# Performance work log

Hardware: AMD Instinct MI355X
Metric: run time of the kernel (lower is better)

## Reference

```python
import jax, jax.numpy as jnp
import numpy as np

B, N, D, P = 32, 16, 64, 8  # batch, num_objs, in_feat_dim, patch size
PAIRS = N * (N - 1)


def _conv_relu(x, W, b):
    # Conv2d(kernel=3, stride=1, padding=1) + ReLU, NCHW/OIHW layout
    y = jax.lax.conv_general_dilated(
        x, W, window_strides=(1, 1), padding='SAME',
        dimension_numbers=('NCHW', 'OIHW', 'NCHW'))
    return jax.nn.relu(y + b[None, :, None, None])


def setup_inputs() -> dict:
    key = jax.random.key(0)
    ks = jax.random.split(key, 12)
    x = jax.random.normal(ks[0], (B, N, D, P, P), jnp.float32)
    # g_idx: cols 0,1 index into the repeated pair axis of size N*(N-1); col 2 is a 0/1 mask
    i0 = jax.random.randint(ks[1], (B, PAIRS, 1), 0, PAIRS)
    i1 = jax.random.randint(ks[2], (B, PAIRS, 1), 0, PAIRS)
    m = jax.random.randint(ks[3], (B, PAIRS, 1), 0, 2)
    g_idx = jnp.concatenate([i0, i1, m], axis=2)

    def w(k, o, i):
        return jax.random.normal(k, (o, i, 3, 3), jnp.float32) * (1.0 / np.sqrt(i * 9.0))

    return {
        'x': x, 'g_idx': g_idx,
        'W_rel': w(ks[4], D, 2 * D), 'b_rel': jnp.zeros((D,), jnp.float32),
        'W_self': w(ks[5], D, D), 'b_self': jnp.zeros((D,), jnp.float32),
        'W_aff': w(ks[6], D, D), 'b_aff': jnp.zeros((D,), jnp.float32),
        'W_agg': w(ks[7], D, 2 * D), 'b_agg': jnp.zeros((D,), jnp.float32),
    }


def reference(x, g_idx, W_rel, b_rel, W_self, b_self, W_aff, b_aff, W_agg, b_agg):
    b, n, d, p, _ = x.shape
    pairs = n * (n - 1)
    s = x
    # x1: [B, N*(N-1), D, P, P]
    x1 = jnp.tile(x, (1, n - 1, 1, 1, 1))

    def gather_pair(col):
        idx = g_idx[:, :, col][:, :, None, None, None]  # [B, pairs, 1, 1, 1]
        idx = jnp.broadcast_to(idx, (b, pairs, d, p, p))
        return jnp.take_along_axis(x1, idx, axis=1)

    y1 = gather_pair(0)
    y2 = gather_pair(1)
    mask = g_idx[:, :, 2][:, :, None, None, None].astype(x.dtype)
    r = jnp.concatenate([y1, y2], axis=2) * mask  # [B, pairs, 2D, P, P]
    r = _conv_relu(r.reshape(-1, 2 * d, p, p), W_rel, b_rel)
    r = r.reshape(b, n, n - 1, d, p, p).sum(axis=2)  # scatter-sum per object

    xs = _conv_relu(x.reshape(-1, d, p, p), W_self, b_self).reshape(b, n, d, p, p)
    pred = xs + r
    a = _conv_relu(pred.reshape(-1, d, p, p), W_aff, b_aff).reshape(b, n, d, p, p)
    a = jnp.concatenate([a, s], axis=2)  # [B, N, 2D, P, P]
    out = _conv_relu(a.reshape(-1, 2 * d, p, p), W_agg, b_agg).reshape(b, n, d, p, p)
    return out
```

## Files before the change

kernel.cpp:

```cpp
#include <hip/hip_runtime.h>


#define NIMG 512
#define IMGSZ 4096

using bf16x8 = __attribute__((ext_vector_type(8))) short;
using f32x4  = __attribute__((ext_vector_type(4))) float;
using u16x8  = __attribute__((ext_vector_type(8))) unsigned short;

__device__ inline unsigned short f2bf(float f) {
  union { float f; unsigned u; } v; v.f = f;
  unsigned r = v.u + 0x7fffu + ((v.u >> 16) & 1u);
  return (unsigned short)(r >> 16);
}

__global__ __launch_bounds__(256) void prep(
    const float* __restrict__ x,
    const float* __restrict__ Wr, const float* __restrict__ Ws,
    const float* __restrict__ Wa, const float* __restrict__ Wg,
    unsigned short* __restrict__ xt, unsigned short* __restrict__ Wt)
{
  const int blk = blockIdx.x;
  if (blk < 512) {
    __shared__ __align__(16) unsigned short st[64 * 68];
    const int tid = threadIdx.x, w = tid >> 6, lane = tid & 63;
    const float* base = x + (size_t)blk * IMGSZ;
    const int px = lane;
#pragma unroll
    for (int r = 0; r < 8; ++r) {
      int ic0 = (w + 4 * r) * 2;
      const float* s = base + ic0 * 64;
      float a = s[px], c = s[64 + px];
      *(unsigned*)(st + px * 68 + ic0) = (unsigned)f2bf(a) | ((unsigned)f2bf(c) << 16);
    }
    __syncthreads();
    const int row = tid >> 2;
#pragma unroll
    for (int k = 0; k < 2; ++k) {
      int c = (tid & 3) * 2 + k;
      *(u16x8*)(xt + (size_t)blk * IMGSZ + row * 64 + c * 8) =
          *(const u16x8*)(st + row * 68 + c * 8);
    }
  } else {
    int idx = (blk - 512) * 256 + threadIdx.x;
    if (idx >= 221184) return;
    float v;
    if (idx < 73728) {
      int c = idx / 36864, r = idx % 36864;
      int t = r >> 12, oc = (r >> 6) & 63, ic = r & 63;
      v = (c == 0 ? Ws : Wa)[oc * 576 + ic * 9 + t];
    } else {
      int r2 = idx - 73728;
      int half = r2 / 73728, rr = r2 % 73728;
      int t = rr >> 13, oc = (rr >> 7) & 63, ic = rr & 127;
      v = (half ? Wg : Wr)[oc * 1152 + ic * 9 + t];
    }
    Wt[idx] = f2bf(v);
  }
}

__device__ inline void decode_img(int j, int& b, int& o) {
  b = ((j >> 7) << 3) | (j & 7);
  o = (j >> 3) & 15;
}

__global__ __launch_bounds__(256) void k1(
    const unsigned short* __restrict__ xt,
    const unsigned short* __restrict__ Wt,
    const float* __restrict__ b_self,
    float* __restrict__ xs, float* __restrict__ cA, float* __restrict__ cB)
{
  constexpr int ROW = 72;
  __shared__ __align__(16) unsigned short sX[65 * ROW];
  int b, o;
  decode_img(blockIdx.x, b, o);
  const int img = b * 16 + o;
  const int tid = threadIdx.x;
  const int w = tid >> 6, lane = tid & 63;

  {
    const unsigned short* xo = xt + (size_t)img * IMGSZ;
    const int row = tid >> 2, c = tid & 3;
    *(u16x8*)(sX + row * ROW + c * 16)     = *(const u16x8*)(xo + row * 64 + c * 16);
    *(u16x8*)(sX + row * ROW + c * 16 + 8) = *(const u16x8*)(xo + row * 64 + c * 16 + 8);
  }
  if (tid < 36) ((unsigned*)(sX + 64 * ROW))[tid] = 0;
  __syncthreads();

  const int q = lane >> 4, n16 = lane & 15;
  const int ocb = w * 16;
  const int co = ocb + q * 4;
  const int aw64 = (ocb + n16) * 64 + q * 8;

  int pyt[4], pxt[4];
#pragma unroll
  for (int t = 0; t < 4; ++t) { int p = t * 16 + n16; pyt[t] = p >> 3; pxt[t] = p & 7; }

  f32x4 aS[4] = {}, aA[4] = {}, aB[4] = {};
  const unsigned short* WS = Wt + aw64;
  const unsigned short* WA = Wt + 73728 + (ocb + n16) * 128 + q * 8;
  const unsigned short* WB = WA + 64;
#pragma unroll
  for (int tap = 0; tap < 9; ++tap) {
    const int dy = tap / 3 - 1, dx = tap % 3 - 1;
    int spt[4];
#pragma unroll
    for (int t = 0; t < 4; ++t) {
      int sy = pyt[t] + dy, sx = pxt[t] + dx;
      spt[t] = ((unsigned)sy < 8u && (unsigned)sx < 8u) ? (sy * 8 + sx) : 64;
    }
#pragma unroll
    for (int ks = 0; ks < 2; ++ks) {
      bf16x8 as = *(const bf16x8*)(WS + tap * 4096 + ks * 32);
      bf16x8 aa = *(const bf16x8*)(WA + tap * 8192 + ks * 32);
      bf16x8 ab = *(const bf16x8*)(WB + tap * 8192 + ks * 32);
#pragma unroll
      for (int t = 0; t < 4; ++t) {
        bf16x8 bt = *(const bf16x8*)(sX + spt[t] * ROW + ks * 32 + q * 8);
        aS[t] = __builtin_amdgcn_mfma_f32_16x16x32_bf16(as, bt, aS[t], 0, 0, 0);
        aA[t] = __builtin_amdgcn_mfma_f32_16x16x32_bf16(aa, bt, aA[t], 0, 0, 0);
        aB[t] = __builtin_amdgcn_mfma_f32_16x16x32_bf16(ab, bt, aB[t], 0, 0, 0);
      }
    }
  }

  const size_t ib = (size_t)img * IMGSZ;
#pragma unroll
  for (int t = 0; t < 4; ++t) {
    int p = t * 16 + n16;
    f32x4 vs = aS[t];
#pragma unroll
    for (int r = 0; r < 4; ++r) vs[r] = fmaxf(vs[r] + b_self[co + r], 0.f);
    *(f32x4*)(xs + ib + p * 64 + co) = vs;
    *(f32x4*)(cA + ib + p * 64 + co) = aA[t];
    *(f32x4*)(cB + ib + p * 64 + co) = aB[t];
  }
}

__global__ __launch_bounds__(256, 2) void k2(
    const unsigned short* __restrict__ xt,
    const int* __restrict__ g_idx,
    const unsigned short* __restrict__ Wt,
    const float* __restrict__ b_rel, const float* __restrict__ b_aff,
    const float* __restrict__ b_agg,
    const float* __restrict__ xs, const float* __restrict__ cA,
    const float* __restrict__ cB,
    float* __restrict__ out)
{
  constexpr int ROW = 72, ROW2 = 136;
  __shared__ __align__(16) unsigned short sX[65 * ROW2];
  __shared__ __align__(16) unsigned short sPred[65 * ROW];
  __shared__ int so1[15], so2[15];
  __shared__ float sm[15];

  int b, i;
  decode_img(blockIdx.x, b, i);
  const int img = b * 16 + i;
  const int tid = threadIdx.x;
  const int w = tid >> 6, lane = tid & 63;

  if (tid < 15) {
    const int* gp = g_idx + ((size_t)b * 240 + i * 15 + tid) * 3;
    so1[tid] = gp[0] & 15;
    so2[tid] = gp[1] & 15;
    sm[tid]  = (float)gp[2];
  }

  {
    const unsigned short* xo = xt + (size_t)img * IMGSZ;
    const int row = tid >> 2, c = tid & 3;
    *(u16x8*)(sX + row * ROW2 + 64 + c * 16)     = *(const u16x8*)(xo + row * 64 + c * 16);
    *(u16x8*)(sX + row * ROW2 + 64 + c * 16 + 8) = *(const u16x8*)(xo + row * 64 + c * 16 + 8);
  }
  if (tid < 68) ((unsigned*)(sX + 64 * ROW2))[tid] = 0;
  if (tid < 36) ((unsigned*)(sPred + 64 * ROW))[tid] = 0;
  __syncthreads();

  {
    const size_t bb = (size_t)b * 16 * IMGSZ;
    const float* xbase = xs + (size_t)img * IMGSZ;
#pragma unroll 1
    for (int pass = 0; pass < 4; ++pass) {
      const int e = tid * 4 + pass * 1024;
      const int e_px = e >> 6, e_ic = e & 63;
      f32x4 v1[15], v2[15];
#pragma unroll
      for (int j = 0; j < 15; ++j) {
        v1[j] = *(const f32x4*)(cA + bb + (size_t)so1[j] * IMGSZ + e);
        v2[j] = *(const f32x4*)(cB + bb + (size_t)so2[j] * IMGSZ + e);
      }
      f32x4 xv = *(const f32x4*)(xbase + e);
      float acc[4], br[4];
#pragma unroll
      for (int r = 0; r < 4; ++r) { br[r] = b_rel[e_ic + r]; acc[r] = xv[r]; }
#pragma unroll
      for (int j = 0; j < 15; ++j) {
        float m = sm[j];
#pragma unroll
        for (int r = 0; r < 4; ++r)
          acc[r] += fmaxf(m * (v1[j][r] + v2[j][r]) + br[r], 0.f);
      }
      uint2 pk;
      pk.x = (unsigned)f2bf(acc[0]) | ((unsigned)f2bf(acc[1]) << 16);
      pk.y = (unsigned)f2bf(acc[2]) | ((unsigned)f2bf(acc[3]) << 16);
      *(uint2*)(sPred + e_px * ROW + e_ic) = pk;
    }
  }
  __syncthreads();

  const int q = lane >> 4, n16 = lane & 15;
  const int ocb = w * 16;
  const int co = ocb + q * 4;
  const int aw64  = (ocb + n16) * 64 + q * 8;
  const int aw128 = (ocb + n16) * 128 + q * 8;

  int pyt[4], pxt[4];
#pragma unroll
  for (int t = 0; t < 4; ++t) { int p = t * 16 + n16; pyt[t] = p >> 3; pxt[t] = p & 7; }

  {
    f32x4 f[4] = {};
    const unsigned short* WA = Wt + 36864 + aw64;
#pragma unroll
    for (int tap = 0; tap < 9; ++tap) {
      const int dy = tap / 3 - 1, dx = tap % 3 - 1;
      int spt[4];
#pragma unroll
      for (int t = 0; t < 4; ++t) {
        int sy = pyt[t] + dy, sx = pxt[t] + dx;
        spt[t] = ((unsigned)sy < 8u && (unsigned)sx < 8u) ? (sy * 8 + sx) : 64;
      }
#pragma unroll
      for (int ks = 0; ks < 2; ++ks) {
        bf16x8 a = *(const bf16x8*)(WA + tap * 4096 + ks * 32);
#pragma unroll
        for (int t = 0; t < 4; ++t) {
          bf16x8 bt = *(const bf16x8*)(sPred + spt[t] * ROW + ks * 32 + q * 8);
          f[t] = __builtin_amdgcn_mfma_f32_16x16x32_bf16(a, bt, f[t], 0, 0, 0);
        }
      }
    }
#pragma unroll
    for (int t = 0; t < 4; ++t) {
      int p = t * 16 + n16;
      float v0 = fmaxf(f[t][0] + b_aff[co + 0], 0.f);
      float v1 = fmaxf(f[t][1] + b_aff[co + 1], 0.f);
      float v2 = fmaxf(f[t][2] + b_aff[co + 2], 0.f);
      float v3 = fmaxf(f[t][3] + b_aff[co + 3], 0.f);
      uint2 pk;
      pk.x = (unsigned)f2bf(v0) | ((unsigned)f2bf(v1) << 16);
      pk.y = (unsigned)f2bf(v2) | ((unsigned)f2bf(v3) << 16);
      *(uint2*)(sX + p * ROW2 + co) = pk;
    }
  }
  __syncthreads();

  {
    f32x4 g[4] = {};
    const unsigned short* WG = Wt + 147456 + aw128;
#pragma unroll
    for (int tap = 0; tap < 9; ++tap) {
      const int dy = tap / 3 - 1, dx = tap % 3 - 1;
      int spt[4];
#pragma unroll
      for (int t = 0; t < 4; ++t) {
        int sy = pyt[t] + dy, sx = pxt[t] + dx;
        spt[t] = ((unsigned)sy < 8u && (unsigned)sx < 8u) ? (sy * 8 + sx) : 64;
      }
#pragma unroll
      for (int ks = 0; ks < 4; ++ks) {
        bf16x8 a = *(const bf16x8*)(WG + tap * 8192 + ks * 32);
#pragma unroll
        for (int t = 0; t < 4; ++t) {
          bf16x8 bt = *(const bf16x8*)(sX + spt[t] * ROW2 + ks * 32 + q * 8);
          g[t] = __builtin_amdgcn_mfma_f32_16x16x32_bf16(a, bt, g[t], 0, 0, 0);
        }
      }
    }
    float* ob = out + (size_t)img * IMGSZ;
#pragma unroll
    for (int t = 0; t < 4; ++t) {
      int p = t * 16 + n16;
#pragma unroll
      for (int r = 0; r < 4; ++r)
        ob[(co + r) * 64 + p] = fmaxf(g[t][r] + b_agg[co + r], 0.f);
    }
  }
}

extern "C" void kernel_launch(void* const* d_in, const int* in_sizes, int n_in,
                              void* d_out, int out_size, void* d_ws, size_t ws_size,
                              hipStream_t stream) {
  const float* x      = (const float*)d_in[0];
  const int*   g_idx  = (const int*)  d_in[1];
  const float* W_rel  = (const float*)d_in[2];
  const float* b_rel  = (const float*)d_in[3];
  const float* W_self = (const float*)d_in[4];
  const float* b_self = (const float*)d_in[5];
  const float* W_aff  = (const float*)d_in[6];
  const float* b_aff  = (const float*)d_in[7];
  const float* W_agg  = (const float*)d_in[8];
  const float* b_agg  = (const float*)d_in[9];
  float* out = (float*)d_out;

  float* ws = (float*)d_ws;
  float* xs = ws;
  float* cA = ws + 2097152;
  float* cB = ws + 2 * 2097152;
  unsigned short* xt = (unsigned short*)(ws + 3 * 2097152);
  unsigned short* Wt = xt + 2097152;

  prep<<<512 + 864, 256, 0, stream>>>(x, W_rel, W_self, W_aff, W_agg, xt, Wt);
  k1<<<NIMG, 256, 0, stream>>>(xt, Wt, b_self, xs, cA, cB);
  k2<<<NIMG, 256, 0, stream>>>(xt, g_idx, Wt, b_rel, b_aff, b_agg,
                               xs, cA, cB, out);
}
```

Measured before the change: 124.5 us.

## Fuse x transpose into conv kernels and move self-conv into k2

The separate x-to-bf16 transpose pass in the prep kernel is removed. k1 and k2 now read fp32 x directly and convert it into shared memory. The self-conv (W_self plus ReLU) moves from k1 into k2, where its result stays in shared memory instead of going through a global xs buffer. This drops a global round trip for xs and for xt, but k2 gains extra MFMA work and LDS usage, which may lower occupancy under its two-blocks-per-SM launch bound.

```diff
diff --git a/kernel.cpp b/kernel.cpp
--- a/kernel.cpp
+++ b/kernel.cpp
@@ -14,49 +14,25 @@
   return (unsigned short)(r >> 16);
 }
 
-__global__ __launch_bounds__(256) void prep(
-    const float* __restrict__ x,
+__global__ __launch_bounds__(256) void prep_w(
     const float* __restrict__ Wr, const float* __restrict__ Ws,
     const float* __restrict__ Wa, const float* __restrict__ Wg,
-    unsigned short* __restrict__ xt, unsigned short* __restrict__ Wt)
+    unsigned short* __restrict__ Wt)
 {
-  const int blk = blockIdx.x;
-  if (blk < 512) {
-    __shared__ __align__(16) unsigned short st[64 * 68];
-    const int tid = threadIdx.x, w = tid >> 6, lane = tid & 63;
-    const float* base = x + (size_t)blk * IMGSZ;
-    const int px = lane;
-#pragma unroll
-    for (int r = 0; r < 8; ++r) {
-      int ic0 = (w + 4 * r) * 2;
-      const float* s = base + ic0 * 64;
-      float a = s[px], c = s[64 + px];
-      *(unsigned*)(st + px * 68 + ic0) = (unsigned)f2bf(a) | ((unsigned)f2bf(c) << 16);
-    }
-    __syncthreads();
-    const int row = tid >> 2;
-#pragma unroll
-    for (int k = 0; k < 2; ++k) {
-      int c = (tid & 3) * 2 + k;
-      *(u16x8*)(xt + (size_t)blk * IMGSZ + row * 64 + c * 8) =
-          *(const u16x8*)(st + row * 68 + c * 8);
-    }
+  int idx = blockIdx.x * 256 + threadIdx.x;
+  if (idx >= 221184) return;
+  float v;
+  if (idx < 73728) {
+    int c = idx / 36864, r = idx % 36864;
+    int t = r >> 12, oc = (r >> 6) & 63, ic = r & 63;
+    v = (c == 0 ? Ws : Wa)[oc * 576 + ic * 9 + t];
   } else {
-    int idx = (blk - 512) * 256 + threadIdx.x;
-    if (idx >= 221184) return;
-    float v;
-    if (idx < 73728) {
-      int c = idx / 36864, r = idx % 36864;
-      int t = r >> 12, oc = (r >> 6) & 63, ic = r & 63;
-      v = (c == 0 ? Ws : Wa)[oc * 576 + ic * 9 + t];
-    } else {
-      int r2 = idx - 73728;
-      int half = r2 / 73728, rr = r2 % 73728;
-      int t = rr >> 13, oc = (rr >> 7) & 63, ic = rr & 127;
-      v = (half ? Wg : Wr)[oc * 1152 + ic * 9 + t];
-    }
-    Wt[idx] = f2bf(v);
-  }
+    int r2 = idx - 73728;
+    int half = r2 / 73728, rr = r2 % 73728;
+    int t = rr >> 13, oc = (rr >> 7) & 63, ic = rr & 127;
+    v = (half ? Wg : Wr)[oc * 1152 + ic * 9 + t];
+  }
+  Wt[idx] = f2bf(v);
 }
 
 __device__ inline void decode_img(int j, int& b, int& o) {
@@ -64,11 +40,24 @@
   o = (j >> 3) & 15;
 }
 
+template<int ROWX>
+__device__ inline void stage_x(const float* __restrict__ xb,
+                               unsigned short* __restrict__ s,
+                               int coff, int w, int px) {
+#pragma unroll
+  for (int r = 0; r < 8; ++r) {
+    int ic0 = (w + 4 * r) * 2;
+    const float* sp = xb + ic0 * 64;
+    float a = sp[px], c = sp[64 + px];
+    *(unsigned*)(s + px * ROWX + coff + ic0) =
+        (unsigned)f2bf(a) | ((unsigned)f2bf(c) << 16);
+  }
+}
+
 __global__ __launch_bounds__(256) void k1(
-    const unsigned short* __restrict__ xt,
+    const float* __restrict__ x,
     const unsigned short* __restrict__ Wt,
-    const float* __restrict__ b_self,
-    float* __restrict__ xs, float* __restrict__ cA, float* __restrict__ cB)
+    float* __restrict__ cA, float* __restrict__ cB)
 {
   constexpr int ROW = 72;
   __shared__ __align__(16) unsigned short sX[65 * ROW];
@@ -78,26 +67,19 @@
   const int tid = threadIdx.x;
   const int w = tid >> 6, lane = tid & 63;
 
-  {
-    const unsigned short* xo = xt + (size_t)img * IMGSZ;
-    const int row = tid >> 2, c = tid & 3;
-    *(u16x8*)(sX + row * ROW + c * 16)     = *(const u16x8*)(xo + row * 64 + c * 16);
-    *(u16x8*)(sX + row * ROW + c * 16 + 8) = *(const u16x8*)(xo + row * 64 + c * 16 + 8);
-  }
+  stage_x<ROW>(x + (size_t)img * IMGSZ, sX, 0, w, lane);
   if (tid < 36) ((unsigned*)(sX + 64 * ROW))[tid] = 0;
   __syncthreads();
 
   const int q = lane >> 4, n16 = lane & 15;
   const int ocb = w * 16;
   const int co = ocb + q * 4;
-  const int aw64 = (ocb + n16) * 64 + q * 8;
 
   int pyt[4], pxt[4];
 #pragma unroll
   for (int t = 0; t < 4; ++t) { int p = t * 16 + n16; pyt[t] = p >> 3; pxt[t] = p & 7; }
 
-  f32x4 aS[4] = {}, aA[4] = {}, aB[4] = {};
-  const unsigned short* WS = Wt + aw64;
+  f32x4 aA[4] = {}, aB[4] = {};
   const unsigned short* WA = Wt + 73728 + (ocb + n16) * 128 + q * 8;
   const unsigned short* WB = WA + 64;
 #pragma unroll
@@ -111,13 +93,11 @@
     }
 #pragma unroll
     for (int ks = 0; ks < 2; ++ks) {
-      bf16x8 as = *(const bf16x8*)(WS + tap * 4096 + ks * 32);
       bf16x8 aa = *(const bf16x8*)(WA + tap * 8192 + ks * 32);
       bf16x8 ab = *(const bf16x8*)(WB + tap * 8192 + ks * 32);
 #pragma unroll
       for (int t = 0; t < 4; ++t) {
         bf16x8 bt = *(const bf16x8*)(sX + spt[t] * ROW + ks * 32 + q * 8);
-        aS[t] = __builtin_amdgcn_mfma_f32_16x16x32_bf16(as, bt, aS[t], 0, 0, 0);
         aA[t] = __builtin_amdgcn_mfma_f32_16x16x32_bf16(aa, bt, aA[t], 0, 0, 0);
         aB[t] = __builtin_amdgcn_mfma_f32_16x16x32_bf16(ab, bt, aB[t], 0, 0, 0);
       }
@@ -128,28 +108,24 @@
 #pragma unroll
   for (int t = 0; t < 4; ++t) {
     int p = t * 16 + n16;
-    f32x4 vs = aS[t];
-#pragma unroll
-    for (int r = 0; r < 4; ++r) vs[r] = fmaxf(vs[r] + b_self[co + r], 0.f);
-    *(f32x4*)(xs + ib + p * 64 + co) = vs;
     *(f32x4*)(cA + ib + p * 64 + co) = aA[t];
     *(f32x4*)(cB + ib + p * 64 + co) = aB[t];
   }
 }
 
 __global__ __launch_bounds__(256, 2) void k2(
-    const unsigned short* __restrict__ xt,
+    const float* __restrict__ x,
     const int* __restrict__ g_idx,
     const unsigned short* __restrict__ Wt,
-    const float* __restrict__ b_rel, const float* __restrict__ b_aff,
-    const float* __restrict__ b_agg,
-    const float* __restrict__ xs, const float* __restrict__ cA,
-    const float* __restrict__ cB,
+    const float* __restrict__ b_rel, const float* __restrict__ b_self,
+    const float* __restrict__ b_aff, const float* __restrict__ b_agg,
+    const float* __restrict__ cA, const float* __restrict__ cB,
     float* __restrict__ out)
 {
-  constexpr int ROW = 72, ROW2 = 136;
+  constexpr int ROW = 72, ROW2 = 136, XROW = 68;
   __shared__ __align__(16) unsigned short sX[65 * ROW2];
   __shared__ __align__(16) unsigned short sPred[65 * ROW];
+  __shared__ __align__(16) float sXS[64 * XROW];
   __shared__ int so1[15], so2[15];
   __shared__ float sm[15];
 
@@ -166,19 +142,56 @@
     sm[tid]  = (float)gp[2];
   }
 
-  {
-    const unsigned short* xo = xt + (size_t)img * IMGSZ;
-    const int row = tid >> 2, c = tid & 3;
-    *(u16x8*)(sX + row * ROW2 + 64 + c * 16)     = *(const u16x8*)(xo + row * 64 + c * 16);
-    *(u16x8*)(sX + row * ROW2 + 64 + c * 16 + 8) = *(const u16x8*)(xo + row * 64 + c * 16 + 8);
-  }
+  stage_x<ROW2>(x + (size_t)img * IMGSZ, sX, 64, w, lane);
   if (tid < 68) ((unsigned*)(sX + 64 * ROW2))[tid] = 0;
   if (tid < 36) ((unsigned*)(sPred + 64 * ROW))[tid] = 0;
   __syncthreads();
 
+  const int q = lane >> 4, n16 = lane & 15;
+  const int ocb = w * 16;
+  const int co = ocb + q * 4;
+  const int aw64  = (ocb + n16) * 64 + q * 8;
+  const int aw128 = (ocb + n16) * 128 + q * 8;
+
+  int pyt[4], pxt[4];
+#pragma unroll
+  for (int t = 0; t < 4; ++t) { int p = t * 16 + n16; pyt[t] = p >> 3; pxt[t] = p & 7; }
+
+  {
+    f32x4 f[4] = {};
+    const unsigned short* WS = Wt + aw64;
+#pragma unroll
+    for (int tap = 0; tap < 9; ++tap) {
+      const int dy = tap / 3 - 1, dx = tap % 3 - 1;
+      int spt[4];
+#pragma unroll
+      for (int t = 0; t < 4; ++t) {
+        int sy = pyt[t] + dy, sx = pxt[t] + dx;
+        spt[t] = ((unsigned)sy < 8u && (unsigned)sx < 8u) ? (sy * 8 + sx) : 64;
+      }
+#pragma unroll
+      for (int ks = 0; ks < 2; ++ks) {
+        bf16x8 a = *(const bf16x8*)(WS + tap * 4096 + ks * 32);
+#pragma unroll
+        for (int t = 0; t < 4; ++t) {
+          bf16x8 bt = *(const bf16x8*)(sX + spt[t] * ROW2 + 64 + ks * 32 + q * 8);
+          f[t] = __builtin_amdgcn_mfma_f32_16x16x32_bf16(a, bt, f[t], 0, 0, 0);
+        }
+      }
+    }
+#pragma unroll
+    for (int t = 0; t < 4; ++t) {
+      int p = t * 16 + n16;
+      f32x4 vs = f[t];
+#pragma unroll
+      for (int r = 0; r < 4; ++r) vs[r] = fmaxf(vs[r] + b_self[co + r], 0.f);
+      *(f32x4*)(sXS + p * XROW + co) = vs;
+    }
+  }
+  __syncthreads();
+
   {
     const size_t bb = (size_t)b * 16 * IMGSZ;
-    const float* xbase = xs + (size_t)img * IMGSZ;
 #pragma unroll 1
     for (int pass = 0; pass < 4; ++pass) {
       const int e = tid * 4 + pass * 1024;
@@ -189,7 +202,7 @@
         v1[j] = *(const f32x4*)(cA + bb + (size_t)so1[j] * IMGSZ + e);
         v2[j] = *(const f32x4*)(cB + bb + (size_t)so2[j] * IMGSZ + e);
       }
-      f32x4 xv = *(const f32x4*)(xbase + e);
+      f32x4 xv = *(const f32x4*)(sXS + e_px * XROW + e_ic);
       float acc[4], br[4];
 #pragma unroll
       for (int r = 0; r < 4; ++r) { br[r] = b_rel[e_ic + r]; acc[r] = xv[r]; }
@@ -207,16 +220,6 @@
     }
   }
   __syncthreads();
-
-  const int q = lane >> 4, n16 = lane & 15;
-  const int ocb = w * 16;
-  const int co = ocb + q * 4;
-  const int aw64  = (ocb + n16) * 64 + q * 8;
-  const int aw128 = (ocb + n16) * 128 + q * 8;
-
-  int pyt[4], pxt[4];
-#pragma unroll
-  for (int t = 0; t < 4; ++t) { int p = t * 16 + n16; pyt[t] = p >> 3; pxt[t] = p & 7; }
 
   {
     f32x4 f[4] = {};
@@ -304,14 +307,12 @@
   float* out = (float*)d_out;
 
   float* ws = (float*)d_ws;
-  float* xs = ws;
-  float* cA = ws + 2097152;
-  float* cB = ws + 2 * 2097152;
-  unsigned short* xt = (unsigned short*)(ws + 3 * 2097152);
-  unsigned short* Wt = xt + 2097152;
-
-  prep<<<512 + 864, 256, 0, stream>>>(x, W_rel, W_self, W_aff, W_agg, xt, Wt);
-  k1<<<NIMG, 256, 0, stream>>>(xt, Wt, b_self, xs, cA, cB);
-  k2<<<NIMG, 256, 0, stream>>>(xt, g_idx, Wt, b_rel, b_aff, b_agg,
-                               xs, cA, cB, out);
-}
+  float* cA = ws;
+  float* cB = ws + 2097152;
+  unsigned short* Wt = (unsigned short*)(ws + 2 * 2097152);
+
+  prep_w<<<864, 256, 0, stream>>>(W_rel, W_self, W_aff, W_agg, Wt);
+  k1<<<NIMG, 256, 0, stream>>>(x, Wt, cA, cB);
+  k2<<<NIMG, 256, 0, stream>>>(x, g_idx, Wt, b_rel, b_self, b_aff, b_agg,
+                               cA, cB, out);
+}
```

After: 122.6 us. Within noise of the previous version (-1.5%).
